# Kernel tuning notes

Hardware: AMD Instinct MI355X
Metric: run time of the kernel (lower is better)

## Reference

```python
import jax, jax.numpy as jnp
import numpy as np

N, E, D, H, Z = 100000, 1600000, 128, 256, 64


def _gconv(x, src, dst, W, b, n):
    # DGL GraphConv, norm='both': D_in^{-1/2} A D_out^{-1/2} x W + b
    ones = jnp.ones(src.shape, x.dtype)
    deg_out = jnp.clip(jax.ops.segment_sum(ones, src, num_segments=n), 1.0)
    deg_in = jnp.clip(jax.ops.segment_sum(ones, dst, num_segments=n), 1.0)
    h = x * (deg_out ** -0.5)[:, None]          # scale by src out-degree
    agg = jax.ops.segment_sum(h[src], dst, num_segments=n)  # SpMM gather/scatter
    return (agg * (deg_in ** -0.5)[:, None]) @ W + b


def setup_inputs() -> dict:
    key = jax.random.key(0)
    ks = jax.random.split(key, 8)
    return {
        "features": jax.random.normal(ks[0], (N, D), jnp.float32),
        "src": jax.random.randint(ks[1], (E,), 0, N, jnp.int32),
        "dst": jax.random.randint(ks[2], (E,), 0, N, jnp.int32),
        "eps": jax.random.normal(ks[3], (N, Z), jnp.float32),
        "W1": jax.random.normal(ks[4], (D, H), jnp.float32) * (1.0 / np.sqrt(D)),
        "b1": jnp.zeros((H,), jnp.float32),
        "W2": jax.random.normal(ks[5], (H, 2 * Z), jnp.float32) * (1.0 / np.sqrt(H)),
        "b2": jnp.zeros((2 * Z,), jnp.float32),
        "W3": jax.random.normal(ks[6], (Z, D), jnp.float32) * (1.0 / np.sqrt(Z)),
        "b3": jnp.zeros((D,), jnp.float32),
    }


def reference(features, src, dst, eps, W1, b1, W2, b2, W3, b3):
    n = features.shape[0]
    h = jax.nn.relu(_gconv(features, src, dst, W1, b1, n))
    mean_logvar = _gconv(h, src, dst, W2, b2, n)
    mean, log_var = jnp.split(mean_logvar, 2, axis=1)
    z = eps * jnp.exp(0.5 * log_var) + mean  # reparameterization
    recon = _gconv(z, src, dst, W3, b3, n)
    return recon, mean, log_var
```

## Files before the change

### kernel.cpp

```cpp
#include <hip/hip_runtime.h>
#include <math.h>


#define MAXD 64
#define FBSH 8
#define EPT  16

typedef short short8 __attribute__((ext_vector_type(8)));
typedef float f32x4 __attribute__((ext_vector_type(4)));

__device__ __forceinline__ unsigned short f2bf(float f) {
  union { float f; unsigned u; } c; c.f = f;
  unsigned r = c.u + 0x7FFF + ((c.u >> 16) & 1);
  return (unsigned short)(r >> 16);
}
__device__ __forceinline__ float bf2f(unsigned short b) {
  return __builtin_bit_cast(float, (unsigned)b << 16);
}
__device__ __forceinline__ void acc8(float* a, uint4 p) {
  a[0] += __builtin_bit_cast(float, p.x << 16);
  a[1] += __builtin_bit_cast(float, p.x & 0xFFFF0000u);
  a[2] += __builtin_bit_cast(float, p.y << 16);
  a[3] += __builtin_bit_cast(float, p.y & 0xFFFF0000u);
  a[4] += __builtin_bit_cast(float, p.z << 16);
  a[5] += __builtin_bit_cast(float, p.z & 0xFFFF0000u);
  a[6] += __builtin_bit_cast(float, p.w << 16);
  a[7] += __builtin_bit_cast(float, p.w & 0xFFFF0000u);
}

__global__ __launch_bounds__(256) void k_bucket2(const int* __restrict__ src,
    const int* __restrict__ dst, int* __restrict__ bcd, int* __restrict__ bcs,
    int* __restrict__ bktd, unsigned char* __restrict__ srec,
    int E, int NFB, int cap2) {
  extern __shared__ int sh[];
  int* lcd = sh;
  int* lbd = sh + NFB;
  int* lcs = sh + 2 * NFB;
  int* lbs = sh + 3 * NFB;
  int tid = threadIdx.x;
  for (int i = tid; i < 4 * NFB; i += 256) sh[i] = 0;
  __syncthreads();
  int e0 = blockIdx.x * (256 * EPT);
  #pragma unroll 4
  for (int j = 0; j < EPT; j++) {
    int e = e0 + j * 256 + tid;
    if (e < E) {
      int d = dst[e]; atomicAdd(&lcd[d >> FBSH], 1);
      int s = src[e]; atomicAdd(&lcs[s >> FBSH], 1);
    }
  }
  __syncthreads();
  for (int fb = tid; fb < NFB; fb += 256) {
    int c = lcd[fb];
    if (c) lbd[fb] = atomicAdd(&bcd[fb], c);
    int cs = lcs[fb];
    if (cs) lbs[fb] = atomicAdd(&bcs[fb], cs);
  }
  __syncthreads();
  #pragma unroll 4
  for (int j = 0; j < EPT; j++) {
    int e = e0 + j * 256 + tid;
    if (e < E) {
      int d = dst[e]; int s = src[e];
      int fbd = d >> FBSH;
      int od = atomicAdd(&lbd[fbd], 1);
      if (od < cap2) bktd[(size_t)fbd * cap2 + od] = ((d & 255) << 24) | s;
      int fbs = s >> FBSH;
      int os = atomicAdd(&lbs[fbs], 1);
      if (os < cap2) srec[(size_t)fbs * cap2 + os] = (unsigned char)(s & 255);
    }
  }
}

__global__ __launch_bounds__(256) void k_csrdeg(const int* __restrict__ bktd,
    const int* __restrict__ bcd, const unsigned char* __restrict__ srec,
    const int* __restrict__ bcs, int* __restrict__ cnt, float* __restrict__ sin_,
    float* __restrict__ sout, int* __restrict__ ebuf, int N, int cap2) {
  __shared__ int lcnt[256];
  __shared__ int lh[256];
  int fb = blockIdx.x;
  int tid = threadIdx.x;
  lcnt[tid] = 0;
  lh[tid] = 0;
  __syncthreads();
  {
    int m = bcd[fb]; m = m < cap2 ? m : cap2;
    const int* rec = bktd + (size_t)fb * cap2;
    for (int i0 = tid * 4; i0 < m; i0 += 1024) {
      if (i0 + 4 <= m) {
        int4 r = *(const int4*)(rec + i0);
        int dl, s, p;
        dl = (unsigned)r.x >> 24; s = r.x & 0xFFFFFF;
        p = atomicAdd(&lcnt[dl], 1);
        if (p < MAXD) ebuf[((size_t)(fb << FBSH) + dl) * MAXD + p] = s;
        dl = (unsigned)r.y >> 24; s = r.y & 0xFFFFFF;
        p = atomicAdd(&lcnt[dl], 1);
        if (p < MAXD) ebuf[((size_t)(fb << FBSH) + dl) * MAXD + p] = s;
        dl = (unsigned)r.z >> 24; s = r.z & 0xFFFFFF;
        p = atomicAdd(&lcnt[dl], 1);
        if (p < MAXD) ebuf[((size_t)(fb << FBSH) + dl) * MAXD + p] = s;
        dl = (unsigned)r.w >> 24; s = r.w & 0xFFFFFF;
        p = atomicAdd(&lcnt[dl], 1);
        if (p < MAXD) ebuf[((size_t)(fb << FBSH) + dl) * MAXD + p] = s;
      } else {
        for (int k = i0; k < m; k++) {
          int r = rec[k];
          int dl = (unsigned)r >> 24; int s = r & 0xFFFFFF;
          int p = atomicAdd(&lcnt[dl], 1);
          if (p < MAXD) ebuf[((size_t)(fb << FBSH) + dl) * MAXD + p] = s;
        }
      }
    }
  }
  {
    int m = bcs[fb]; m = m < cap2 ? m : cap2;
    const unsigned char* rec = srec + (size_t)fb * cap2;
    for (int i0 = tid * 4; i0 < m; i0 += 1024) {
      if (i0 + 4 <= m) {
        uchar4 r = *(const uchar4*)(rec + i0);
        atomicAdd(&lh[r.x], 1); atomicAdd(&lh[r.y], 1);
        atomicAdd(&lh[r.z], 1); atomicAdd(&lh[r.w], 1);
      } else {
        for (int k = i0; k < m; k++) atomicAdd(&lh[rec[k]], 1);
      }
    }
  }
  __syncthreads();
  int node = (fb << FBSH) + tid;
  if (node < N) {
    int c = lcnt[tid];
    cnt[node] = c;
    sin_[node] = rsqrtf((float)(c < 1 ? 1 : c));
    int d = lh[tid];
    sout[node] = rsqrtf((float)(d < 1 ? 1 : d));
  }
}

__global__ __launch_bounds__(256) void k_cvt(const float* __restrict__ in,
    const float* __restrict__ sout, unsigned short* __restrict__ out, int n) {
  int i = (blockIdx.x * 256 + threadIdx.x) * 4;
  if (i >= n) return;
  float s = sout[i >> 7];
  float4 f = *(const float4*)(in + i);
  unsigned lo = (unsigned)f2bf(s * f.x) | ((unsigned)f2bf(s * f.y) << 16);
  unsigned hi = (unsigned)f2bf(s * f.z) | ((unsigned)f2bf(s * f.w) << 16);
  uint2 o; o.x = lo; o.y = hi;
  *(uint2*)(out + i) = o;
}

template <int K, int OC>
__device__ __forceinline__ void wrepack_body(const float* __restrict__ W,
    short* __restrict__ Wp, int t) {
  constexpr int KC = K / 32;
  int lane = t & 63;
  int kc = (t >> 6) % KC;
  int nt = t / (KC * 64);
  int n = nt * 16 + (lane & 15);
  int k0 = kc * 32 + ((lane >> 4) * 8);
  short8 v;
  #pragma unroll
  for (int j = 0; j < 8; j++) v[j] = (short)f2bf(W[(size_t)(k0 + j) * OC + n]);
  *(short8*)(Wp + (size_t)t * 8) = v;
}

__global__ __launch_bounds__(256) void k_wrepack_all(
    const float* __restrict__ W1, const float* __restrict__ W2,
    const float* __restrict__ W3, short* __restrict__ W1p,
    short* __restrict__ W2p, short* __restrict__ W3p) {
  int t = blockIdx.x * 256 + threadIdx.x;
  if (t < 4096) wrepack_body<128, 256>(W1, W1p, t);
  else if (t < 8192) wrepack_body<256, 128>(W2, W2p, t - 4096);
  else if (t < 9216) wrepack_body<64, 128>(W3, W3p, t - 8192);
}

template <int K, int OC, bool RELU, bool BIAS, bool OUTBF16, bool SOUT>
__global__ __launch_bounds__(256) void k_gemm_mfma(
    const unsigned short* __restrict__ A, const short* __restrict__ Wp,
    const float* __restrict__ bias, const float* __restrict__ srow,
    void* __restrict__ Cout, int N) {
  constexpr int KC = K / 32;
  constexpr int NT = OC / 16;
  int lane = threadIdx.x & 63;
  int wv = threadIdx.x >> 6;
  int m0 = (blockIdx.x * 4 + wv) * 16;
  if (m0 >= N) return;
  int mrow = m0 + (lane & 15);
  if (mrow >= N) mrow = N - 1;
  int q = lane >> 4;
  short8 av[KC];
  #pragma unroll
  for (int kc = 0; kc < KC; kc++)
    av[kc] = *(const short8*)(A + (size_t)mrow * K + kc * 32 + q * 8);
  int col0 = lane & 15;
  int rbase = m0 + q * 4;
  float sr[4];
  if (SOUT) {
    #pragma unroll
    for (int r = 0; r < 4; r++) {
      int row = rbase + r;
      sr[r] = (row < N) ? srow[row] : 1.f;
    }
  }
  #pragma unroll
  for (int nt = 0; nt < NT; nt++) {
    f32x4 acc = {0.f, 0.f, 0.f, 0.f};
    #pragma unroll
    for (int kc = 0; kc < KC; kc++) {
      short8 bv = *(const short8*)(Wp + ((size_t)(nt * KC + kc) * 64 + lane) * 8);
      acc = __builtin_amdgcn_mfma_f32_16x16x32_bf16(av[kc], bv, acc, 0, 0, 0);
    }
    int col = nt * 16 + col0;
    float bb = BIAS ? bias[col] : 0.f;
    #pragma unroll
    for (int r = 0; r < 4; r++) {
      int row = rbase + r;
      if (row < N) {
        float v = acc[r] + bb;
        if (RELU) v = fmaxf(v, 0.f);
        if (SOUT) v *= sr[r];
        if (OUTBF16) ((unsigned short*)Cout)[(size_t)row * OC + col] = f2bf(v);
        else         ((float*)Cout)[(size_t)row * OC + col] = v;
      }
    }
  }
}

__global__ __launch_bounds__(256) void k_spmm128v(const unsigned short* __restrict__ x,
    const int* __restrict__ ebuf, const int* __restrict__ cnt,
    const float* __restrict__ sin_, unsigned short* __restrict__ out, int N) {
  int lane = threadIdx.x & 63;
  int v = blockIdx.x * 4 + (threadIdx.x >> 6);
  if (v >= N) return;
  v = __builtin_amdgcn_readfirstlane(v);
  int c = cnt[v]; c = c < MAXD ? c : MAXD;
  const int* el = ebuf + (size_t)v * MAXD;
  int u_l = (lane < c) ? el[lane] : 0;
  int q = lane >> 4;
  int fo = (lane & 15) * 8;
  float a[8] = {0, 0, 0, 0, 0, 0, 0, 0};
  int i = 0;
  for (; i + 16 <= c; i += 16) {
    int u0 = __shfl(u_l, i + q);
    int u1 = __shfl(u_l, i + 4 + q);
    int u2 = __shfl(u_l, i + 8 + q);
    int u3 = __shfl(u_l, i + 12 + q);
    uint4 p0 = *(const uint4*)(x + (size_t)u0 * 128 + fo);
    uint4 p1 = *(const uint4*)(x + (size_t)u1 * 128 + fo);
    uint4 p2 = *(const uint4*)(x + (size_t)u2 * 128 + fo);
    uint4 p3 = *(const uint4*)(x + (size_t)u3 * 128 + fo);
    acc8(a, p0); acc8(a, p1); acc8(a, p2); acc8(a, p3);
  }
  for (; i + 8 <= c; i += 8) {
    int u0 = __shfl(u_l, i + q);
    int u1 = __shfl(u_l, i + 4 + q);
    uint4 p0 = *(const uint4*)(x + (size_t)u0 * 128 + fo);
    uint4 p1 = *(const uint4*)(x + (size_t)u1 * 128 + fo);
    acc8(a, p0); acc8(a, p1);
  }
  for (; i < c; i += 4) {
    int eidx = i + q;
    int u = __shfl(u_l, eidx);
    uint4 p = *(const uint4*)(x + (size_t)u * 128 + fo);
    if (eidx >= c) { p.x = 0; p.y = 0; p.z = 0; p.w = 0; }
    acc8(a, p);
  }
  #pragma unroll
  for (int j = 0; j < 8; j++) {
    a[j] += __shfl_xor(a[j], 16);
    a[j] += __shfl_xor(a[j], 32);
  }
  if (lane < 16) {
    float sv = sin_[v];
    uint4 o;
    o.x = (unsigned)f2bf(sv * a[0]) | ((unsigned)f2bf(sv * a[1]) << 16);
    o.y = (unsigned)f2bf(sv * a[2]) | ((unsigned)f2bf(sv * a[3]) << 16);
    o.z = (unsigned)f2bf(sv * a[4]) | ((unsigned)f2bf(sv * a[5]) << 16);
    o.w = (unsigned)f2bf(sv * a[6]) | ((unsigned)f2bf(sv * a[7]) << 16);
    *(uint4*)(out + (size_t)v * 128 + fo) = o;
  }
}

__global__ __launch_bounds__(256) void k_spmm2v(const unsigned short* __restrict__ hw,
    const int* __restrict__ ebuf, const int* __restrict__ cnt,
    const float* __restrict__ sout, const float* __restrict__ sin_,
    const float* __restrict__ b2, const float* __restrict__ eps,
    float* __restrict__ mean_out, float* __restrict__ logvar_out,
    unsigned short* __restrict__ z, int N) {
  int lane = threadIdx.x & 63;
  int v = blockIdx.x * 4 + (threadIdx.x >> 6);
  if (v >= N) return;
  v = __builtin_amdgcn_readfirstlane(v);
  int c = cnt[v]; c = c < MAXD ? c : MAXD;
  const int* el = ebuf + (size_t)v * MAXD;
  int u_l = (lane < c) ? el[lane] : 0;
  int q = lane >> 4;
  int fo = (lane & 15) * 8;
  float a[8] = {0, 0, 0, 0, 0, 0, 0, 0};
  int i = 0;
  for (; i + 16 <= c; i += 16) {
    int u0 = __shfl(u_l, i + q);
    int u1 = __shfl(u_l, i + 4 + q);
    int u2 = __shfl(u_l, i + 8 + q);
    int u3 = __shfl(u_l, i + 12 + q);
    uint4 p0 = *(const uint4*)(hw + (size_t)u0 * 128 + fo);
    uint4 p1 = *(const uint4*)(hw + (size_t)u1 * 128 + fo);
    uint4 p2 = *(const uint4*)(hw + (size_t)u2 * 128 + fo);
    uint4 p3 = *(const uint4*)(hw + (size_t)u3 * 128 + fo);
    acc8(a, p0); acc8(a, p1); acc8(a, p2); acc8(a, p3);
  }
  for (; i + 8 <= c; i += 8) {
    int u0 = __shfl(u_l, i + q);
    int u1 = __shfl(u_l, i + 4 + q);
    uint4 p0 = *(const uint4*)(hw + (size_t)u0 * 128 + fo);
    uint4 p1 = *(const uint4*)(hw + (size_t)u1 * 128 + fo);
    acc8(a, p0); acc8(a, p1);
  }
  for (; i < c; i += 4) {
    int eidx = i + q;
    int u = __shfl(u_l, eidx);
    uint4 p = *(const uint4*)(hw + (size_t)u * 128 + fo);
    if (eidx >= c) { p.x = 0; p.y = 0; p.z = 0; p.w = 0; }
    acc8(a, p);
  }
  #pragma unroll
  for (int j = 0; j < 8; j++) {
    a[j] += __shfl_xor(a[j], 16);
    a[j] += __shfl_xor(a[j], 32);
  }
  float sv = sin_[v];
  float4 blo = *(const float4*)(b2 + fo);
  float4 bhi = *(const float4*)(b2 + fo + 4);
  float m[8];
  m[0] = fmaf(sv, a[0], blo.x); m[1] = fmaf(sv, a[1], blo.y);
  m[2] = fmaf(sv, a[2], blo.z); m[3] = fmaf(sv, a[3], blo.w);
  m[4] = fmaf(sv, a[4], bhi.x); m[5] = fmaf(sv, a[5], bhi.y);
  m[6] = fmaf(sv, a[6], bhi.z); m[7] = fmaf(sv, a[7], bhi.w);
  float lv[8];
  #pragma unroll
  for (int j = 0; j < 8; j++) lv[j] = __shfl_xor(m[j], 8);
  int k = lane & 15;
  if (lane < 16) {
    if (k < 8) {
      *(float4*)(mean_out + (size_t)v * 64 + k * 8) =
          make_float4(m[0], m[1], m[2], m[3]);
      *(float4*)(mean_out + (size_t)v * 64 + k * 8 + 4) =
          make_float4(m[4], m[5], m[6], m[7]);
      float so = sout[v];
      float4 e0 = *(const float4*)(eps + (size_t)v * 64 + k * 8);
      float4 e1 = *(const float4*)(eps + (size_t)v * 64 + k * 8 + 4);
      float z0 = so * fmaf(e0.x, expf(0.5f * lv[0]), m[0]);
      float z1 = so * fmaf(e0.y, expf(0.5f * lv[1]), m[1]);
      float z2 = so * fmaf(e0.z, expf(0.5f * lv[2]), m[2]);
      float z3 = so * fmaf(e0.w, expf(0.5f * lv[3]), m[3]);
      float z4 = so * fmaf(e1.x, expf(0.5f * lv[4]), m[4]);
      float z5 = so * fmaf(e1.y, expf(0.5f * lv[5]), m[5]);
      float z6 = so * fmaf(e1.z, expf(0.5f * lv[6]), m[6]);
      float z7 = so * fmaf(e1.w, expf(0.5f * lv[7]), m[7]);
      uint4 o;
      o.x = (unsigned)f2bf(z0) | ((unsigned)f2bf(z1) << 16);
      o.y = (unsigned)f2bf(z2) | ((unsigned)f2bf(z3) << 16);
      o.z = (unsigned)f2bf(z4) | ((unsigned)f2bf(z5) << 16);
      o.w = (unsigned)f2bf(z6) | ((unsigned)f2bf(z7) << 16);
      *(uint4*)(z + (size_t)v * 64 + k * 8) = o;
    } else {
      *(float4*)(logvar_out + (size_t)v * 64 + (k - 8) * 8) =
          make_float4(m[0], m[1], m[2], m[3]);
      *(float4*)(logvar_out + (size_t)v * 64 + (k - 8) * 8 + 4) =
          make_float4(m[4], m[5], m[6], m[7]);
    }
  }
}

__global__ __launch_bounds__(256) void k_spmm64v(const unsigned short* __restrict__ z,
    const int* __restrict__ ebuf, const int* __restrict__ cnt,
    const float* __restrict__ sin_, unsigned short* __restrict__ aggz, int N) {
  int lane = threadIdx.x & 63;
  int v = blockIdx.x * 4 + (threadIdx.x >> 6);
  if (v >= N) return;
  v = __builtin_amdgcn_readfirstlane(v);
  int c = cnt[v]; c = c < MAXD ? c : MAXD;
  const int* el = ebuf + (size_t)v * MAXD;
  int u_l = (lane < c) ? el[lane] : 0;
  int o8 = lane >> 3;
  int fo = (lane & 7) * 8;
  float a[8] = {0, 0, 0, 0, 0, 0, 0, 0};
  int i = 0;
  for (; i + 32 <= c; i += 32) {
    int u0 = __shfl(u_l, i + o8);
    int u1 = __shfl(u_l, i + 8 + o8);
    int u2 = __shfl(u_l, i + 16 + o8);
    int u3 = __shfl(u_l, i + 24 + o8);
    uint4 p0 = *(const uint4*)(z + (size_t)u0 * 64 + fo);
    uint4 p1 = *(const uint4*)(z + (size_t)u1 * 64 + fo);
    uint4 p2 = *(const uint4*)(z + (size_t)u2 * 64 + fo);
    uint4 p3 = *(const uint4*)(z + (size_t)u3 * 64 + fo);
    acc8(a, p0); acc8(a, p1); acc8(a, p2); acc8(a, p3);
  }
  for (; i + 16 <= c; i += 16) {
    int u0 = __shfl(u_l, i + o8);
    int u1 = __shfl(u_l, i + 8 + o8);
    uint4 p0 = *(const uint4*)(z + (size_t)u0 * 64 + fo);
    uint4 p1 = *(const uint4*)(z + (size_t)u1 * 64 + fo);
    acc8(a, p0); acc8(a, p1);
  }
  for (; i < c; i += 8) {
    int eidx = i + o8;
    int u = __shfl(u_l, eidx);
    uint4 p = *(const uint4*)(z + (size_t)u * 64 + fo);
    if (eidx >= c) { p.x = 0; p.y = 0; p.z = 0; p.w = 0; }
    acc8(a, p);
  }
  #pragma unroll
  for (int j = 0; j < 8; j++) {
    a[j] += __shfl_xor(a[j], 8);
    a[j] += __shfl_xor(a[j], 16);
    a[j] += __shfl_xor(a[j], 32);
  }
  if (lane < 8) {
    float sv = sin_[v];
    uint4 o;
    o.x = (unsigned)f2bf(sv * a[0]) | ((unsigned)f2bf(sv * a[1]) << 16);
    o.y = (unsigned)f2bf(sv * a[2]) | ((unsigned)f2bf(sv * a[3]) << 16);
    o.z = (unsigned)f2bf(sv * a[4]) | ((unsigned)f2bf(sv * a[5]) << 16);
    o.w = (unsigned)f2bf(sv * a[6]) | ((unsigned)f2bf(sv * a[7]) << 16);
    *(uint4*)(aggz + (size_t)v * 64 + fo) = o;
  }
}

extern "C" void kernel_launch(void* const* d_in, const int* in_sizes, int n_in,
                              void* d_out, int out_size, void* d_ws, size_t ws_size,
                              hipStream_t stream) {
  const float* features = (const float*)d_in[0];
  const int*   src      = (const int*)d_in[1];
  const int*   dst      = (const int*)d_in[2];
  const float* eps      = (const float*)d_in[3];
  const float* W1       = (const float*)d_in[4];
  const float* b1       = (const float*)d_in[5];
  const float* W2       = (const float*)d_in[6];
  const float* b2       = (const float*)d_in[7];
  const float* W3       = (const float*)d_in[8];
  const float* b3       = (const float*)d_in[9];
  const int E = in_sizes[1];
  const int N = in_sizes[3] / 64;
  float* out = (float*)d_out;

  const int NFB = (N + 255) >> FBSH;
  const int cap2 = ((E / NFB) + 2048 + 255) & ~255;

  char* ws = (char*)d_ws;
  int* cnt    = (int*)ws;            ws += (size_t)N * 4;
  int* bcd    = (int*)ws;            ws += (size_t)NFB * 4;
  int* bcs    = (int*)ws;            ws += (size_t)NFB * 4;
  int* ebuf   = (int*)ws;            ws += (size_t)N * MAXD * 4;
  float* sout = (float*)ws;          ws += (size_t)N * 4;
  float* sin_ = (float*)ws;          ws += (size_t)N * 4;
  short* W1p  = (short*)ws;          ws += 128 * 256 * 2;
  short* W2p  = (short*)ws;          ws += 256 * 128 * 2;
  short* W3p  = (short*)ws;          ws += 64 * 128 * 2;
  char* R1    = ws;                  ws += (size_t)N * 256;
  char* R2    = ws;                  ws += (size_t)N * 256;

  unsigned short* xb    = (unsigned short*)R1;
  unsigned short* hwb   = (unsigned short*)R1;
  unsigned short* aggzb = (unsigned short*)R1;
  unsigned short* agg1b = (unsigned short*)R2;
  unsigned short* zb    = (unsigned short*)R2;
  int* bktd = (int*)R2;
  unsigned char* srec = (unsigned char*)(R2 + (size_t)NFB * cap2 * 4);

  unsigned short* h     = (unsigned short*)out;
  float* recon          = out;
  float* mean_out       = out + (size_t)N * 128;
  float* logvar_out     = out + (size_t)N * 192;

  hipMemsetAsync(bcd, 0, (size_t)NFB * 8, stream);

  const size_t shA = (size_t)4 * NFB * 4;
  k_bucket2<<<(E + 256 * EPT - 1) / (256 * EPT), 256, shA, stream>>>(
      src, dst, bcd, bcs, bktd, srec, E, NFB, cap2);
  k_csrdeg<<<NFB, 256, 0, stream>>>(bktd, bcd, srec, bcs, cnt, sin_, sout,
                                    ebuf, N, cap2);
  k_cvt<<<((N * 128 / 4) + 255) / 256, 256, 0, stream>>>(features, sout, xb, N * 128);
  k_wrepack_all<<<36, 256, 0, stream>>>(W1, W2, W3, W1p, W2p, W3p);

  k_spmm128v<<<(N + 3) / 4, 256, 0, stream>>>(xb, ebuf, cnt, sin_, agg1b, N);
  k_gemm_mfma<128, 256, true, true, true, true>
      <<<(N + 63) / 64, 256, 0, stream>>>(agg1b, W1p, b1, sout, h, N);

  k_gemm_mfma<256, 128, false, false, true, false>
      <<<(N + 63) / 64, 256, 0, stream>>>(h, W2p, nullptr, nullptr, hwb, N);
  k_spmm2v<<<(N + 3) / 4, 256, 0, stream>>>(hwb, ebuf, cnt, sout, sin_, b2, eps,
                                            mean_out, logvar_out, zb, N);

  k_spmm64v<<<(N + 3) / 4, 256, 0, stream>>>(zb, ebuf, cnt, sin_, aggzb, N);
  k_gemm_mfma<64, 128, false, true, false, false>
      <<<(N + 63) / 64, 256, 0, stream>>>(aggzb, W3p, b3, nullptr, recon, N);
}
```

Before: 519.8 us.

## Fuse layer-1 and layer-2 GEMMs through LDS to skip hidden round-trip

The two back-to-back GEMMs (agg1 @ W1 with bias, ReLU and out-degree scaling, then h @ W2) become one kernel. Each wave keeps its 16x256 bf16 hidden tile in shared memory and feeds it directly into the second MFMA GEMM. This removes writing and rereading the N x 256 bf16 hidden tensor in global memory, plus one kernel launch. In exchange each block uses about 33 KB of LDS and needs a block-wide barrier, which may lower occupancy. The generic GEMM template is reduced to the fp32-output case that remains in use.

```diff
diff --git a/kernel.cpp b/kernel.cpp
--- a/kernel.cpp
+++ b/kernel.cpp
@@ -173,11 +173,74 @@
   else if (t < 9216) wrepack_body<64, 128>(W3, W3p, t - 8192);
 }
 
-template <int K, int OC, bool RELU, bool BIAS, bool OUTBF16, bool SOUT>
+__global__ __launch_bounds__(256) void k_gemm12(
+    const unsigned short* __restrict__ A,
+    const short* __restrict__ W1p, const short* __restrict__ W2p,
+    const float* __restrict__ b1, const float* __restrict__ srow,
+    unsigned short* __restrict__ hwb, int N) {
+  __shared__ unsigned short lh[4][16][264];
+  int lane = threadIdx.x & 63;
+  int wv = threadIdx.x >> 6;
+  int m0 = (blockIdx.x * 4 + wv) * 16;
+  bool active = m0 < N;
+  int mrow = m0 + (lane & 15);
+  if (mrow >= N) mrow = N - 1;
+  int q = lane >> 4;
+  int col0 = lane & 15;
+  int rbl = q * 4;
+  if (active) {
+    short8 av[4];
+    #pragma unroll
+    for (int kc = 0; kc < 4; kc++)
+      av[kc] = *(const short8*)(A + (size_t)mrow * 128 + kc * 32 + q * 8);
+    float sr[4];
+    #pragma unroll
+    for (int r = 0; r < 4; r++) {
+      int row = m0 + rbl + r;
+      sr[r] = (row < N) ? srow[row] : 1.f;
+    }
+    #pragma unroll
+    for (int nt = 0; nt < 16; nt++) {
+      f32x4 acc = {0.f, 0.f, 0.f, 0.f};
+      #pragma unroll
+      for (int kc = 0; kc < 4; kc++) {
+        short8 bv = *(const short8*)(W1p + ((size_t)(nt * 4 + kc) * 64 + lane) * 8);
+        acc = __builtin_amdgcn_mfma_f32_16x16x32_bf16(av[kc], bv, acc, 0, 0, 0);
+      }
+      int col = nt * 16 + col0;
+      float bb = b1[col];
+      #pragma unroll
+      for (int r = 0; r < 4; r++)
+        lh[wv][rbl + r][col] = f2bf(fmaxf(acc[r] + bb, 0.f) * sr[r]);
+    }
+  }
+  __syncthreads();
+  if (!active) return;
+  short8 av2[8];
+  #pragma unroll
+  for (int kc = 0; kc < 8; kc++)
+    av2[kc] = *(const short8*)&lh[wv][col0][kc * 32 + q * 8];
+  #pragma unroll
+  for (int nt = 0; nt < 8; nt++) {
+    f32x4 acc = {0.f, 0.f, 0.f, 0.f};
+    #pragma unroll
+    for (int kc = 0; kc < 8; kc++) {
+      short8 bv = *(const short8*)(W2p + ((size_t)(nt * 8 + kc) * 64 + lane) * 8);
+      acc = __builtin_amdgcn_mfma_f32_16x16x32_bf16(av2[kc], bv, acc, 0, 0, 0);
+    }
+    int col = nt * 16 + col0;
+    #pragma unroll
+    for (int r = 0; r < 4; r++) {
+      int row = m0 + rbl + r;
+      if (row < N) hwb[(size_t)row * 128 + col] = f2bf(acc[r]);
+    }
+  }
+}
+
+template <int K, int OC, bool BIAS>
 __global__ __launch_bounds__(256) void k_gemm_mfma(
     const unsigned short* __restrict__ A, const short* __restrict__ Wp,
-    const float* __restrict__ bias, const float* __restrict__ srow,
-    void* __restrict__ Cout, int N) {
+    const float* __restrict__ bias, float* __restrict__ Cout, int N) {
   constexpr int KC = K / 32;
   constexpr int NT = OC / 16;
   int lane = threadIdx.x & 63;
@@ -193,14 +256,6 @@
     av[kc] = *(const short8*)(A + (size_t)mrow * K + kc * 32 + q * 8);
   int col0 = lane & 15;
   int rbase = m0 + q * 4;
-  float sr[4];
-  if (SOUT) {
-    #pragma unroll
-    for (int r = 0; r < 4; r++) {
-      int row = rbase + r;
-      sr[r] = (row < N) ? srow[row] : 1.f;
-    }
-  }
   #pragma unroll
   for (int nt = 0; nt < NT; nt++) {
     f32x4 acc = {0.f, 0.f, 0.f, 0.f};
@@ -214,13 +269,7 @@
     #pragma unroll
     for (int r = 0; r < 4; r++) {
       int row = rbase + r;
-      if (row < N) {
-        float v = acc[r] + bb;
-        if (RELU) v = fmaxf(v, 0.f);
-        if (SOUT) v *= sr[r];
-        if (OUTBF16) ((unsigned short*)Cout)[(size_t)row * OC + col] = f2bf(v);
-        else         ((float*)Cout)[(size_t)row * OC + col] = v;
-      }
+      if (row < N) Cout[(size_t)row * OC + col] = acc[r] + bb;
     }
   }
 }
@@ -468,7 +517,6 @@
   int* bktd = (int*)R2;
   unsigned char* srec = (unsigned char*)(R2 + (size_t)NFB * cap2 * 4);
 
-  unsigned short* h     = (unsigned short*)out;
   float* recon          = out;
   float* mean_out       = out + (size_t)N * 128;
   float* logvar_out     = out + (size_t)N * 192;
@@ -484,15 +532,12 @@
   k_wrepack_all<<<36, 256, 0, stream>>>(W1, W2, W3, W1p, W2p, W3p);
 
   k_spmm128v<<<(N + 3) / 4, 256, 0, stream>>>(xb, ebuf, cnt, sin_, agg1b, N);
-  k_gemm_mfma<128, 256, true, true, true, true>
-      <<<(N + 63) / 64, 256, 0, stream>>>(agg1b, W1p, b1, sout, h, N);
-
-  k_gemm_mfma<256, 128, false, false, true, false>
-      <<<(N + 63) / 64, 256, 0, stream>>>(h, W2p, nullptr, nullptr, hwb, N);
+  k_gemm12<<<(N + 63) / 64, 256, 0, stream>>>(agg1b, W1p, W2p, b1, sout, hwb, N);
+
   k_spmm2v<<<(N + 3) / 4, 256, 0, stream>>>(hwb, ebuf, cnt, sout, sin_, b2, eps,
                                             mean_out, logvar_out, zb, N);
 
   k_spmm64v<<<(N + 3) / 4, 256, 0, stream>>>(zb, ebuf, cnt, sin_, aggzb, N);
-  k_gemm_mfma<64, 128, false, true, false, false>
-      <<<(N + 63) / 64, 256, 0, stream>>>(aggzb, W3p, b3, nullptr, recon, N);
-}
+  k_gemm_mfma<64, 128, true>
+      <<<(N + 63) / 64, 256, 0, stream>>>(aggzb, W3p, b3, recon, N);
+}
```

Result: faster. 501.4 us (-3.6%).
